# Optimization experiments

Hardware: AMD Instinct MI355X
Metric: run time of the kernel (lower is better)

Reference implementation:

```python
import jax, jax.numpy as jnp
import numpy as np
from functools import partial

DIM = 256
HEADS = 8
RED = 4
HEAD_DIM = DIM // HEADS
SCALE = 1.0 / np.sqrt(HEAD_DIM).astype(np.float32)


def _conv(x, w, stride):
    # x: [B, C, H, W], w: [O, I, kh, kw] (OIHW), VALID padding
    return jax.lax.conv_general_dilated(
        x, w, window_strides=(stride, stride), padding='VALID',
        dimension_numbers=('NCHW', 'OIHW', 'NCHW'))


def setup_inputs() -> dict:
    key = jax.random.key(0)
    ks = jax.random.split(key, 5)
    B, H, W = 8, 64, 64
    x = jax.random.normal(ks[0], (B, DIM, H, W), dtype=jnp.float32)
    # conv weights, scaled like default kaiming-ish init
    wq = jax.random.normal(ks[1], (DIM, DIM, 1, 1), dtype=jnp.float32) / np.sqrt(DIM)
    wk = jax.random.normal(ks[2], (DIM, DIM, RED, RED), dtype=jnp.float32) / np.sqrt(DIM * RED * RED)
    wv = jax.random.normal(ks[3], (DIM, DIM, RED, RED), dtype=jnp.float32) / np.sqrt(DIM * RED * RED)
    wout = jax.random.normal(ks[4], (DIM, DIM, 1, 1), dtype=jnp.float32) / np.sqrt(DIM)
    return {"x": x, "wq": wq, "wk": wk, "wv": wv, "wout": wout}


def reference(x, wq, wk, wv, wout):
    B, C, H, W = x.shape
    q = _conv(x, wq, 1)            # [B, C, H, W]
    k = _conv(x, wk, RED)          # [B, C, H/r, W/r]
    v = _conv(x, wv, RED)          # [B, C, H/r, W/r]

    def split_heads(t):
        b, c, h, w = t.shape
        # b (n d) h w -> b n d (h w)
        return t.reshape(b, HEADS, HEAD_DIM, h * w)

    q, k, v = split_heads(q), split_heads(k), split_heads(v)
    # attn: [B, n, i, j], i = H*W, j = (H/r)*(W/r)
    attn = jnp.einsum('bndi,bndj->bnij', q, k) * SCALE
    attn = jax.nn.softmax(attn, axis=-1)
    out = jnp.einsum('bnij,bndj->bndi', attn, v)   # [B, n, d, H*W]
    out = out.reshape(B, C, H, W)                  # b (n d) h w
    return _conv(out, wout, 1)
```

## Files before the change

### kernel.cpp

```cpp
#include <hip/hip_runtime.h>
#include <hip/hip_bf16.h>


typedef __attribute__((ext_vector_type(8))) short s16x8;
typedef __attribute__((ext_vector_type(4))) short s16x4;
typedef __attribute__((ext_vector_type(4))) float f32x4;
typedef __attribute__((ext_vector_type(16))) float f32x16;

#define MFMA16(a,b,c) __builtin_amdgcn_mfma_f32_16x16x32_bf16(a,b,c,0,0,0)
#define MFMA32(a,b,c) __builtin_amdgcn_mfma_f32_32x32x16_bf16(a,b,c,0,0,0)

typedef const __attribute__((address_space(1))) void* gas1_t;
typedef __attribute__((address_space(3))) void* las3_t;

__device__ __forceinline__ unsigned short bfb(float f){
  __hip_bfloat16 h = __float2bfloat16(f);
  return __builtin_bit_cast(unsigned short, h);
}

__device__ __forceinline__ void async16(void* l, const void* g){
  __builtin_amdgcn_global_load_lds((gas1_t)g, (las3_t)l, 16, 0, 0);
}

__global__ __launch_bounds__(256) void k_cvt_w(const float* __restrict__ wq,
                                               const float* __restrict__ wk,
                                               const float* __restrict__ wv,
                                               const float* __restrict__ wo,
                                               unsigned short* __restrict__ dst){
  int c = blockIdx.x*256 + threadIdx.x;
  int e = c*4;
  const float* s; int off;
  if (e < 65536)        { s = wq; off = e; }
  else if (e < 1114112) { s = wk; off = e - 65536; }
  else if (e < 2162688) { s = wv; off = e - 1114112; }
  else                  { s = wo; off = e - 2162688; }
  float4 f = *(const float4*)(s + off);
  s16x4 o; o[0]=(short)bfb(f.x); o[1]=(short)bfb(f.y); o[2]=(short)bfb(f.z); o[3]=(short)bfb(f.w);
  *(s16x4*)(dst + e) = o;
}

__global__ __launch_bounds__(256) void k_cvt_x(const float* __restrict__ x,
                                               unsigned short* __restrict__ xT,
                                               unsigned short* __restrict__ xcolT){
  __shared__ __align__(16) unsigned short lx[32*4*72];
  const int cc = blockIdx.x, hc = blockIdx.y, b = blockIdx.z;
  const int ci0 = cc*32, h0 = hc*4;
  const int t = threadIdx.x;
  #pragma unroll
  for (int s=0; s<8; ++s){
    int c = s*256 + t;
    int ci = c>>6, rem = c&63, kh = rem>>4, wq = rem&15;
    float4 f = *(const float4*)(x + ((size_t)((b*256+ci0+ci)*64 + h0+kh)*64 + wq*4));
    s16x4 o; o[0]=(short)bfb(f.x); o[1]=(short)bfb(f.y); o[2]=(short)bfb(f.z); o[3]=(short)bfb(f.w);
    *(s16x4*)(&lx[(ci*4+kh)*72 + wq*4]) = o;
  }
  __syncthreads();
  {
    int kh = t>>6, w = t&63;
    size_t p = (size_t)(h0+kh)*64 + w;
    unsigned short* dst = xT + ((size_t)b*4096 + p)*256 + ci0;
    s16x8 o[4];
    #pragma unroll
    for (int c2=0;c2<32;c2++) o[c2>>3][c2&7] = (short)lx[(c2*4+kh)*72 + w];
    #pragma unroll
    for (int q2=0;q2<4;q2++) *(s16x8*)(dst + q2*8) = o[q2];
  }
  {
    int w2 = t&15, u = t>>4;
    int pr = hc*16 + w2;
    unsigned short* dst = xcolT + ((size_t)b*256 + pr)*4096 + (ci0 + u*2)*16;
    s16x8 o[4];
    #pragma unroll
    for (int c2=0;c2<2;c2++)
      #pragma unroll
      for (int kh=0;kh<4;kh++)
        #pragma unroll
        for (int kw=0;kw<4;kw++)
          o[c2*2 + (kh>>1)][(kh&1)*4 + kw] = (short)lx[((u*2+c2)*4+kh)*72 + w2*4 + kw];
    #pragma unroll
    for (int q2=0;q2<4;q2++) *(s16x8*)(dst + q2*8) = o[q2];
  }
}

template<int MODE>
__device__ __forceinline__ void gemm_core(const unsigned short* __restrict__ A,
                                          const unsigned short* __restrict__ B,
                                          void* __restrict__ O,
                                          int ldA, int ldB, int ldO,
                                          int m0, int n0, int kOfs, int nK){
  __shared__ __align__(16) unsigned short As[128*32];
  __shared__ __align__(16) unsigned short Bs[128*32];
  const int t = threadIdx.x;
  const int lane = t & 63, wvi = t >> 6;
  const int wm = (wvi>>1)*64, wn = (wvi&1)*64;
  const int g = lane>>4, l15 = lane&15;
  f32x4 acc[4][4];
  #pragma unroll
  for (int i=0;i<4;i++)
    #pragma unroll
    for (int j=0;j<4;j++) acc[i][j] = f32x4{0.f,0.f,0.f,0.f};

  for (int kt=0; kt<nK; ++kt){
    const int k0 = kOfs + kt*32;
    __syncthreads();
    #pragma unroll
    for (int s=0;s<2;s++){
      int chunk = s*256 + t;
      int row = chunk>>2, kq = chunk&3;
      async16(&As[chunk*8], A + (size_t)(m0+row)*ldA + k0 + kq*8);
    }
    #pragma unroll
    for (int s=0;s<2;s++){
      int chunk = s*256 + t;
      int row = chunk>>2, kq = chunk&3;
      async16(&Bs[chunk*8], B + (size_t)(n0+row)*ldB + k0 + kq*8);
    }
    __syncthreads();
    s16x8 af[4], bv[4];
    #pragma unroll
    for (int i=0;i<4;i++) af[i] = *(const s16x8*)(&As[(wm + i*16 + l15)*32 + g*8]);
    #pragma unroll
    for (int j=0;j<4;j++) bv[j] = *(const s16x8*)(&Bs[(wn + j*16 + l15)*32 + g*8]);
    #pragma unroll
    for (int i=0;i<4;i++)
      #pragma unroll
      for (int j=0;j<4;j++)
        acc[i][j] = MFMA16(af[i], bv[j], acc[i][j]);
  }

  if (MODE == 0){
    unsigned short* Ou = (unsigned short*)O;
    #pragma unroll
    for (int i=0;i<4;i++)
      #pragma unroll
      for (int j=0;j<4;j++){
        int mm = m0 + wm + i*16 + g*4;
        int nn = n0 + wn + j*16 + l15;
        #pragma unroll
        for (int r=0;r<4;r++) Ou[(size_t)(mm+r)*ldO + nn] = bfb(acc[i][j][r]);
      }
  } else if (MODE == 1){
    float* Of = (float*)O;
    #pragma unroll
    for (int i=0;i<4;i++)
      #pragma unroll
      for (int j=0;j<4;j++){
        int mm = m0 + wm + i*16 + g*4;
        int nn = n0 + wn + j*16 + l15;
        *(f32x4*)(Of + (size_t)nn*ldO + mm) = acc[i][j];
      }
  } else {
    float* Of = (float*)O;
    #pragma unroll
    for (int i=0;i<4;i++)
      #pragma unroll
      for (int j=0;j<4;j++){
        int mm = m0 + wm + i*16 + g*4;
        int nn = n0 + wn + j*16 + l15;
        #pragma unroll
        for (int r=0;r<4;r++) Of[(size_t)(mm+r)*ldO + nn] = acc[i][j][r];
      }
  }
}

__global__ __launch_bounds__(256,2) void k_gemm_q(const unsigned short* __restrict__ xT,
                                                  const unsigned short* __restrict__ wqb,
                                                  unsigned short* __restrict__ Qt){
  int b = blockIdx.z;
  gemm_core<0>(xT + (size_t)b*1048576, wqb, Qt + (size_t)b*1048576,
               256, 256, 256, blockIdx.y*128, blockIdx.x*128, 0, 8);
}

__global__ __launch_bounds__(256,2) void k_gemm_kv(const unsigned short* __restrict__ wkb,
                                                   const unsigned short* __restrict__ wvb,
                                                   const unsigned short* __restrict__ xcol,
                                                   float* __restrict__ part, int S){
  int zz = blockIdx.z; int s = zz % S; int rest = zz / S; int w = rest & 1, b = rest >> 1;
  const unsigned short* A = w ? wvb : wkb;
  gemm_core<2>(A, xcol + (size_t)b*1048576,
               part + ((size_t)((w*8+b)*S + s))*65536,
               4096, 4096, 256, blockIdx.y*128, blockIdx.x*128, s*(4096/S), 128/S);
}

__global__ __launch_bounds__(256,2) void k_gemm_out(const unsigned short* __restrict__ attnT,
                                                    const unsigned short* __restrict__ wob,
                                                    float* __restrict__ out){
  int b = blockIdx.z;
  gemm_core<1>(attnT + (size_t)b*1048576, wob, out + (size_t)b*1048576,
               256, 256, 4096, blockIdx.y*128, blockIdx.x*128, 0, 8);
}

__global__ __launch_bounds__(256) void k_reduce_kv(const float* __restrict__ part,
                                                   unsigned short* __restrict__ Kt,
                                                   unsigned short* __restrict__ Vv, int S){
  unsigned idx = blockIdx.x*256 + threadIdx.x;
  int j = idx & 255, co = (idx>>8)&255, bb = (idx>>16)&7, w = idx>>19;
  const float* p = part + (size_t)((w*8+bb)*S)*65536 + co*256 + j;
  float sum = 0.f;
  for (int s2=0;s2<S;s2++) sum += p[(size_t)s2*65536];
  if (w==0) Kt[((size_t)bb*256 + j)*256 + co] = bfb(sum);
  else      Vv[((size_t)bb*256 + co)*256 + j] = bfb(sum);
}

__global__ __launch_bounds__(256,3) void k_attn(const unsigned short* __restrict__ Qt,
                                                const unsigned short* __restrict__ Kt,
                                                const unsigned short* __restrict__ Vv,
                                                unsigned short* __restrict__ attnT){
  __shared__ __align__(16) char smem[43008];
  const int xb = blockIdx.x, n = blockIdx.y, b = blockIdx.z;
  const int t = threadIdx.x, wv = t>>6, lane = t&63, hi = lane>>5, l31 = lane&31;
  char* Ks = smem;
  char* Vs = smem + 16384;
  char* Pb = smem + 32768 + wv*2560;
  const float kexp = 0.17677669529663687f * 1.4426950408889634f;

  #pragma unroll
  for (int s=0;s<4;s++){
    int flat = s*256 + t;
    int j = flat>>2, cc = flat&3;
    int gc = cc ^ ((j>>1)&3);
    async16(Ks + flat*16, Kt + ((size_t)b<<16) + j*256 + n*32 + gc*8);
  }
  #pragma unroll
  for (int s=0;s<4;s++){
    int flat = s*256 + t;
    int d = flat>>5, c = flat&31;
    int gc = c ^ (d&7);
    async16(Vs + flat*16, Vv + ((size_t)b<<16) + (size_t)(n*32+d)*256 + gc*8);
  }
  __syncthreads();

  const int swj = (l31>>1)&3;
  const int swv = l31&7;

  #pragma unroll
  for (int it=0; it<2; ++it){
    const int i0 = xb*256 + it*128 + wv*32;
    const s16x8 q0 = *(const s16x8*)(Qt + ((size_t)(b*4096 + i0 + l31))*256 + n*32 + hi*8);
    const s16x8 q1 = *(const s16x8*)(Qt + ((size_t)(b*4096 + i0 + l31))*256 + n*32 + 16 + hi*8);
    f32x16 oacc = {};
    float lsum = 0.f;

    #pragma unroll
    for (int jb=0;jb<8;jb++){
      const int krow = (jb*32 + l31)*64;
      s16x8 kf0 = *(const s16x8*)(Ks + krow + (((0+hi) ^ swj)<<4));
      s16x8 kf1 = *(const s16x8*)(Ks + krow + (((2+hi) ^ swj)<<4));
      f32x16 sS = MFMA32(kf0, q0, (f32x16){});
      sS = MFMA32(kf1, q1, sS);
      float e[16];
      #pragma unroll
      for (int r=0;r<16;r++){ e[r] = exp2f(sS[r]*kexp); lsum += e[r]; }
      #pragma unroll
      for (int q4=0;q4<4;q4++){
        s16x4 w4; w4[0]=(short)bfb(e[4*q4+0]); w4[1]=(short)bfb(e[4*q4+1]);
                  w4[2]=(short)bfb(e[4*q4+2]); w4[3]=(short)bfb(e[4*q4+3]);
        *(s16x4*)(Pb + l31*80 + q4*16 + hi*8) = w4;
      }
      #pragma unroll
      for (int ks=0;ks<2;ks++){
        s16x8 pa = *(const s16x8*)(Pb + l31*80 + ks*32 + hi*16);
        s16x8 vf = *(const s16x8*)(Vs + l31*512 + (((jb*4 + ks*2 + hi) ^ swv)<<4));
        oacc = MFMA32(pa, vf, oacc);
      }
    }
    lsum += __shfl_xor(lsum, 32);
    float rcp = __builtin_amdgcn_rcpf(lsum);
    const int hi4 = hi*4;
    #pragma unroll
    for (int r=0;r<16;r++){
      int i_r = (r&3) + 8*(r>>2) + hi4;
      float sc = __shfl(rcp, i_r);
      attnT[((size_t)(b*4096 + i0 + i_r))*256 + n*32 + l31] = bfb(oacc[r]*sc);
    }
  }
}

extern "C" void kernel_launch(void* const* d_in, const int* in_sizes, int n_in,
                              void* d_out, int out_size, void* d_ws, size_t ws_size,
                              hipStream_t stream){
  (void)in_sizes; (void)n_in; (void)out_size;
  const float* x    = (const float*)d_in[0];
  const float* wq   = (const float*)d_in[1];
  const float* wk   = (const float*)d_in[2];
  const float* wv   = (const float*)d_in[3];
  const float* wout = (const float*)d_in[4];
  char* ws = (char*)d_ws;

  unsigned short* wb    = (unsigned short*)(ws + 0);
  unsigned short* xT    = (unsigned short*)(ws + 4456448);
  unsigned short* xcol  = (unsigned short*)(ws + 21233664);
  unsigned short* Qt    = (unsigned short*)(ws + 38010880);
  unsigned short* Kt    = (unsigned short*)(ws + 54788096);
  unsigned short* Vv    = (unsigned short*)(ws + 55836672);
  unsigned short* attnT = (unsigned short*)(ws + 21233664);
  float* out = (float*)d_out;

  const size_t part8_off = 56885248ull;
  const size_t part8_end = part8_off + 2ull*8*8*65536*4;
  int S; float* part;
  if (ws_size >= part8_end) { S = 8; part = (float*)(ws + part8_off); }
  else                      { S = 4; part = (float*)(ws + 4456448); }

  unsigned short* wqb = wb;
  unsigned short* wkb = wb + 65536;
  unsigned short* wvb = wb + 1114112;
  unsigned short* wob = wb + 2162688;

  k_cvt_w   <<<2176,            256, 0, stream>>>(wq, wk, wv, wout, wb);
  k_cvt_x   <<<dim3(8,16,8),    256, 0, stream>>>(x, xT, xcol);
  k_gemm_q  <<<dim3(2,32,8),    256, 0, stream>>>(xT, wqb, Qt);
  k_gemm_kv <<<dim3(2,2,16*S),  256, 0, stream>>>(wkb, wvb, xcol, part, S);
  k_reduce_kv<<<4096,           256, 0, stream>>>(part, Kt, Vv, S);
  k_attn    <<<dim3(16,8,8),    256, 0, stream>>>(Qt, Kt, Vv, attnT);
  k_gemm_out<<<dim3(2,32,8),    256, 0, stream>>>(attnT, wob, out);
}
```

Baseline: 183.0 us.

## Merge prep and QKV GEMM launches; stage output GEMM stores through LDS

```diff
diff --git a/kernel.cpp b/kernel.cpp
--- a/kernel.cpp
+++ b/kernel.cpp
@@ -22,37 +22,38 @@
   __builtin_amdgcn_global_load_lds((gas1_t)g, (las3_t)l, 16, 0, 0);
 }
 
-__global__ __launch_bounds__(256) void k_cvt_w(const float* __restrict__ wq,
-                                               const float* __restrict__ wk,
-                                               const float* __restrict__ wv,
-                                               const float* __restrict__ wo,
-                                               unsigned short* __restrict__ dst){
-  int c = blockIdx.x*256 + threadIdx.x;
-  int e = c*4;
-  const float* s; int off;
-  if (e < 65536)        { s = wq; off = e; }
-  else if (e < 1114112) { s = wk; off = e - 65536; }
-  else if (e < 2162688) { s = wv; off = e - 1114112; }
-  else                  { s = wo; off = e - 2162688; }
-  float4 f = *(const float4*)(s + off);
-  s16x4 o; o[0]=(short)bfb(f.x); o[1]=(short)bfb(f.y); o[2]=(short)bfb(f.z); o[3]=(short)bfb(f.w);
-  *(s16x4*)(dst + e) = o;
-}
-
-__global__ __launch_bounds__(256) void k_cvt_x(const float* __restrict__ x,
-                                               unsigned short* __restrict__ xT,
-                                               unsigned short* __restrict__ xcolT){
+__global__ __launch_bounds__(256) void k_prep(const float* __restrict__ wq,
+                                              const float* __restrict__ wk,
+                                              const float* __restrict__ wv,
+                                              const float* __restrict__ wo,
+                                              unsigned short* __restrict__ wb,
+                                              const float* __restrict__ x,
+                                              unsigned short* __restrict__ xT,
+                                              unsigned short* __restrict__ xcolT){
   __shared__ __align__(16) unsigned short lx[32*4*72];
-  const int cc = blockIdx.x, hc = blockIdx.y, b = blockIdx.z;
+  const int bid = blockIdx.x, t = threadIdx.x;
+  if (bid < 2176){
+    int e = (bid*256 + t)*4;
+    const float* s; int off;
+    if (e < 65536)        { s = wq; off = e; }
+    else if (e < 1114112) { s = wk; off = e - 65536; }
+    else if (e < 2162688) { s = wv; off = e - 1114112; }
+    else                  { s = wo; off = e - 2162688; }
+    float4 f = *(const float4*)(s + off);
+    s16x4 o; o[0]=(short)bfb(f.x); o[1]=(short)bfb(f.y); o[2]=(short)bfb(f.z); o[3]=(short)bfb(f.w);
+    *(s16x4*)(wb + e) = o;
+    return;
+  }
+  const int f = bid - 2176;
+  const int cc = f&7, hc = (f>>3)&15, b = f>>7;
   const int ci0 = cc*32, h0 = hc*4;
-  const int t = threadIdx.x;
   #pragma unroll
   for (int s=0; s<8; ++s){
     int c = s*256 + t;
-    int ci = c>>6, rem = c&63, kh = rem>>4, wq = rem&15;
-    float4 f = *(const float4*)(x + ((size_t)((b*256+ci0+ci)*64 + h0+kh)*64 + wq*4));
-    s16x4 o; o[0]=(short)bfb(f.x); o[1]=(short)bfb(f.y); o[2]=(short)bfb(f.z); o[3]=(short)bfb(f.w);
-    *(s16x4*)(&lx[(ci*4+kh)*72 + wq*4]) = o;
+    int ci = c>>6, rem = c&63, kh = rem>>4, wqi = rem&15;
+    float4 fv = *(const float4*)(x + ((size_t)((b*256+ci0+ci)*64 + h0+kh)*64 + wqi*4));
+    s16x4 o; o[0]=(short)bfb(fv.x); o[1]=(short)bfb(fv.y); o[2]=(short)bfb(fv.z); o[3]=(short)bfb(fv.w);
+    *(s16x4*)(&lx[(ci*4+kh)*72 + wqi*4]) = o;
   }
   __syncthreads();
   {
@@ -87,9 +88,8 @@
                                           const unsigned short* __restrict__ B,
                                           void* __restrict__ O,
                                           int ldA, int ldB, int ldO,
-                                          int m0, int n0, int kOfs, int nK){
-  __shared__ __align__(16) unsigned short As[128*32];
-  __shared__ __align__(16) unsigned short Bs[128*32];
+                                          int m0, int n0, int kOfs, int nK,
+                                          unsigned short* As, unsigned short* Bs, float* Cb){
   const int t = threadIdx.x;
   const int lane = t & 63, wvi = t >> 6;
   const int wm = (wvi>>1)*64, wn = (wvi&1)*64;
@@ -139,17 +139,7 @@
         #pragma unroll
         for (int r=0;r<4;r++) Ou[(size_t)(mm+r)*ldO + nn] = bfb(acc[i][j][r]);
       }
-  } else if (MODE == 1){
-    float* Of = (float*)O;
-    #pragma unroll
-    for (int i=0;i<4;i++)
-      #pragma unroll
-      for (int j=0;j<4;j++){
-        int mm = m0 + wm + i*16 + g*4;
-        int nn = n0 + wn + j*16 + l15;
-        *(f32x4*)(Of + (size_t)nn*ldO + mm) = acc[i][j];
-      }
-  } else {
+  } else if (MODE == 2){
     float* Of = (float*)O;
     #pragma unroll
     for (int i=0;i<4;i++)
@@ -160,34 +150,82 @@
         #pragma unroll
         for (int r=0;r<4;r++) Of[(size_t)(mm+r)*ldO + nn] = acc[i][j][r];
       }
+  } else {
+    __syncthreads();
+    float* cw = Cb + wvi*(64*72);
+    #pragma unroll
+    for (int i=0;i<4;i++)
+      #pragma unroll
+      for (int j=0;j<4;j++)
+        *(f32x4*)(cw + (j*16 + l15)*72 + i*16 + g*4) = acc[i][j];
+    float* Of = (float*)O;
+    #pragma unroll
+    for (int ri=0;ri<16;ri++){
+      int co_l = ri*4 + g;
+      int p_l  = l15*4;
+      f32x4 v = *(const f32x4*)(cw + co_l*72 + p_l);
+      *(f32x4*)(Of + (size_t)(n0 + wn + co_l)*ldO + m0 + wm + p_l) = v;
+    }
+  }
+}
+
+__global__ __launch_bounds__(256,2) void k_gemm_qkv(const unsigned short* __restrict__ xT,
+                                                    const unsigned short* __restrict__ wqb,
+                                                    unsigned short* __restrict__ Qt,
+                                                    const unsigned short* __restrict__ wkb,
+                                                    const unsigned short* __restrict__ wvb,
+                                                    const unsigned short* __restrict__ xcol,
+                                                    float* __restrict__ part, int S){
+  __shared__ __align__(16) unsigned short As[128*32];
+  __shared__ __align__(16) unsigned short Bs[128*32];
+  const int bid = blockIdx.x;
+  if (bid < 512){
+    int xg = bid&1, yg = (bid>>1)&31, b = bid>>6;
+    gemm_core<0>(xT + (size_t)b*1048576, wqb, Qt + (size_t)b*1048576,
+                 256, 256, 256, yg*128, xg*128, 0, 8, As, Bs, nullptr);
+  } else {
+    int f2 = bid - 512;
+    int xg = f2&1, yg = (f2>>1)&1, zz = f2>>2;
+    int s = zz % S, rest = zz / S, w = rest & 1, b = rest >> 1;
+    const unsigned short* A = w ? wvb : wkb;
+    gemm_core<2>(A, xcol + (size_t)b*1048576,
+                 part + ((size_t)((w*8+b)*S + s))*65536,
+                 4096, 4096, 256, yg*128, xg*128, s*(4096/S), 128/S, As, Bs, nullptr);
   }
 }
 
 __global__ __launch_bounds__(256,2) void k_gemm_q(const unsigned short* __restrict__ xT,
                                                   const unsigned short* __restrict__ wqb,
                                                   unsigned short* __restrict__ Qt){
+  __shared__ __align__(16) unsigned short As[128*32];
+  __shared__ __align__(16) unsigned short Bs[128*32];
   int b = blockIdx.z;
   gemm_core<0>(xT + (size_t)b*1048576, wqb, Qt + (size_t)b*1048576,
-               256, 256, 256, blockIdx.y*128, blockIdx.x*128, 0, 8);
+               256, 256, 256, blockIdx.y*128, blockIdx.x*128, 0, 8, As, Bs, nullptr);
 }
 
 __global__ __launch_bounds__(256,2) void k_gemm_kv(const unsigned short* __restrict__ wkb,
                                                    const unsigned short* __restrict__ wvb,
                                                    const unsigned short* __restrict__ xcol,
                                                    float* __restrict__ part, int S){
+  __shared__ __align__(16) unsigned short As[128*32];
+  __shared__ __align__(16) unsigned short Bs[128*32];
   int zz = blockIdx.z; int s = zz % S; int rest = zz / S; int w = rest & 1, b = rest >> 1;
   const unsigned short* A = w ? wvb : wkb;
   gemm_core<2>(A, xcol + (size_t)b*1048576,
                part + ((size_t)((w*8+b)*S + s))*65536,
-               4096, 4096, 256, blockIdx.y*128, blockIdx.x*128, s*(4096/S), 128/S);
+               4096, 4096, 256, blockIdx.y*128, blockIdx.x*128, s*(4096/S), 128/S, As, Bs, nullptr);
 }
 
 __global__ __launch_bounds__(256,2) void k_gemm_out(const unsigned short* __restrict__ attnT,
                                                     const unsigned short* __restrict__ wob,
                                                     float* __restrict__ out){
+  __shared__ __align__(16) char smem[73728];
+  unsigned short* As = (unsigned short*)smem;
+  unsigned short* Bs = As + 4096;
   int b = blockIdx.z;
-  gemm_core<1>(attnT + (size_t)b*1048576, wob, out + (size_t)b*1048576,
-               256, 256, 4096, blockIdx.y*128, blockIdx.x*128, 0, 8);
+  gemm_core<3>(attnT + (size_t)b*1048576, wob, out + (size_t)b*1048576,
+               256, 256, 4096, blockIdx.y*128, blockIdx.x*128, 0, 8, As, Bs, (float*)smem);
 }
 
 __global__ __launch_bounds__(256) void k_reduce_kv(const float* __restrict__ part,
@@ -296,22 +334,29 @@
   unsigned short* attnT = (unsigned short*)(ws + 21233664);
   float* out = (float*)d_out;
 
-  const size_t part8_off = 56885248ull;
-  const size_t part8_end = part8_off + 2ull*8*8*65536*4;
-  int S; float* part;
-  if (ws_size >= part8_end) { S = 8; part = (float*)(ws + part8_off); }
-  else                      { S = 4; part = (float*)(ws + 4456448); }
-
   unsigned short* wqb = wb;
   unsigned short* wkb = wb + 65536;
   unsigned short* wvb = wb + 1114112;
   unsigned short* wob = wb + 2162688;
 
-  k_cvt_w   <<<2176,            256, 0, stream>>>(wq, wk, wv, wout, wb);
-  k_cvt_x   <<<dim3(8,16,8),    256, 0, stream>>>(x, xT, xcol);
-  k_gemm_q  <<<dim3(2,32,8),    256, 0, stream>>>(xT, wqb, Qt);
-  k_gemm_kv <<<dim3(2,2,16*S),  256, 0, stream>>>(wkb, wvb, xcol, part, S);
-  k_reduce_kv<<<4096,           256, 0, stream>>>(part, Kt, Vv, S);
-  k_attn    <<<dim3(16,8,8),    256, 0, stream>>>(Qt, Kt, Vv, attnT);
-  k_gemm_out<<<dim3(2,32,8),    256, 0, stream>>>(attnT, wob, out);
-}
+  const size_t part8_off = 56885248ull;
+  const size_t part8_end = part8_off + 2ull*8*8*65536*4;
+
+  k_prep<<<3200, 256, 0, stream>>>(wq, wk, wv, wout, wb, x, xT, xcol);
+
+  if (ws_size >= part8_end){
+    const int S = 8;
+    float* part = (float*)(ws + part8_off);
+    k_gemm_qkv<<<512 + 64*S, 256, 0, stream>>>(xT, wqb, Qt, wkb, wvb, xcol, part, S);
+    k_reduce_kv<<<4096, 256, 0, stream>>>(part, Kt, Vv, S);
+  } else {
+    const int S = 4;
+    float* part = (float*)(ws + 4456448);
+    k_gemm_q <<<dim3(2,32,8),   256, 0, stream>>>(xT, wqb, Qt);
+    k_gemm_kv<<<dim3(2,2,16*S), 256, 0, stream>>>(wkb, wvb, xcol, part, S);
+    k_reduce_kv<<<4096, 256, 0, stream>>>(part, Kt, Vv, S);
+  }
+
+  k_attn    <<<dim3(16,8,8), 256, 0, stream>>>(Qt, Kt, Vv, attnT);
+  k_gemm_out<<<dim3(2,32,8), 256, 0, stream>>>(attnT, wob, out);
+}
```

After: 180.8 us. No clear change (-1.2%).
